# Kernel optimization log

Measured on AMD Instinct MI355X. Metric: run time of the kernel, lower is better.

The kernel has to match this reference:

```python
import jax, jax.numpy as jnp
import numpy as np

NEIGH = (3, 3, 3)  # attn_neighbourhood_size -> 27 one-hot impulse filters


def setup_inputs() -> dict:
    key = jax.random.key(0)
    b, h, d = 2, 8, 32
    H = W = D = 24
    x = jax.random.normal(key, (b, h, H * W * D, d), dtype=jnp.float32)
    return {"x": x, "height": H, "width": W, "depth": D}


def _localize(x, height, width, depth):
    # x: [b, h, N, d] with N = height*width*depth
    b, h, N, d = x.shape
    nh, nw, nd = NEIGH
    ph, pw, pd = (nh - 1) // 2, (nw - 1) // 2, (nd - 1) // 2
    # 'b h (i j k) d -> b h d i j k'
    y = x.reshape(b, h, height, width, depth, d).transpose(0, 1, 5, 2, 3, 4)
    yp = jnp.pad(y, ((0, 0), (0, 0), (0, 0), (ph, ph), (pw, pw), (pd, pd)))
    # conv3d with a unit impulse at (i,j,k) and 'same' padding is exactly the
    # shifted gather out[p] = x_padded[p + (i,j,k)]; emit the 27 shifts directly.
    slices = []
    for i in range(nh):
        for j in range(nw):
            for k in range(nd):
                slices.append(yp[..., i:i + height, j:j + width, k:k + depth])
    # [b, h, d, H, W, D, filter_n]
    out = jnp.stack(slices, axis=-1)
    fn = nh * nw * nd
    # '(b h d) filter_n i j k -> b h (i j k) filter_n d'
    out = out.reshape(b, h, d, N, fn).transpose(0, 1, 3, 4, 2)
    return out


def reference(x, height, width, depth):
    return _localize(x, height, width, depth)
```

## Files before the change

### kernel.cpp

```cpp
#include <hip/hip_runtime.h>


typedef float v4f __attribute__((ext_vector_type(4)));

constexpr int H = 24, W = 24, D = 24;
constexpr int N = H * W * D;
constexpr int FN = 27;
constexpr int BH = 16;
constexpr int N4_REAL = BH * N * FN * 8;

__global__ __launch_bounds__(256) void localize_kernel(
    const v4f* __restrict__ x4, v4f* __restrict__ out4) {
  int idx = blockIdx.x * 256 + threadIdx.x;

  int c4 = idx & 7;
  int t  = idx >> 3;
  int f  = t % FN;
  int t2 = t / FN;
  int n  = t2 % N;

  int ii  = n / (W * D);
  int rem = n % (W * D);
  int jj  = rem / D;
  int kk  = rem % D;

  int di = f / 9 - 1;
  int dj = (f / 3) % 3 - 1;
  int dk = f % 3 - 1;

  int si = ii + di, sj = jj + dj, sk = kk + dk;

  v4f v = (v4f)(0.0f);
  if ((unsigned)si < (unsigned)H && (unsigned)sj < (unsigned)W &&
      (unsigned)sk < (unsigned)D) {
    int delta = di * (W * D) + dj * D + dk;
    v = x4[(t2 + delta) * 8 + c4];
  }
  __builtin_nontemporal_store(v, &out4[idx]);
}

extern "C" void kernel_launch(void* const* d_in, const int* in_sizes, int n_in,
                              void* d_out, int out_size, void* d_ws, size_t ws_size,
                              hipStream_t stream) {
  (void)in_sizes; (void)n_in; (void)out_size; (void)d_ws; (void)ws_size;
  const v4f* x4 = (const v4f*)d_in[0];
  v4f* out4 = (v4f*)d_out;
  int blocks = N4_REAL / 256;
  localize_kernel<<<blocks, 256, 0, stream>>>(x4, out4);
}
```

Before: 802.7 us.

## Stage 3x3 neighbourhood rows in LDS per (bh,i,j) workgroup before scatter

Each workgroup now handles one (bh, i, j) row of depth D. It loads the nine padded source rows (with zero halos) into shared memory, then writes all 27 shifted copies for that row from LDS. The aim is to remove redundant, partly uncoalesced global reads, since each input element was previously read up to 27 times. The cost is an extra barrier and LDS traffic, and a workgroup count that drops to 9216 with a strided loop of about 21 iterations per thread.

```diff
diff --git a/kernel.cpp b/kernel.cpp
--- a/kernel.cpp
+++ b/kernel.cpp
@@ -7,36 +7,48 @@
 constexpr int N = H * W * D;
 constexpr int FN = 27;
 constexpr int BH = 16;
-constexpr int N4_REAL = BH * N * FN * 8;
+constexpr int PLEN = D + 2;
+constexpr int LDS_N4 = 9 * PLEN * 8;
+constexpr int OUT_N4 = D * FN * 8;
 
 __global__ __launch_bounds__(256) void localize_kernel(
     const v4f* __restrict__ x4, v4f* __restrict__ out4) {
-  int idx = blockIdx.x * 256 + threadIdx.x;
+  __shared__ v4f lds[LDS_N4];
+  const int tid = threadIdx.x;
+  const int wg  = blockIdx.x;
+  const int bh  = wg / (H * W);
+  const int rem = wg - bh * (H * W);
+  const int ii  = rem / W;
+  const int jj  = rem - ii * W;
 
-  int c4 = idx & 7;
-  int t  = idx >> 3;
-  int f  = t % FN;
-  int t2 = t / FN;
-  int n  = t2 % N;
+  for (int o = tid; o < LDS_N4; o += 256) {
+    int c4   = o & 7;
+    int r    = o >> 3;
+    int p    = r / PLEN;
+    int srck = r - p * PLEN;
+    int si   = ii + p / 3 - 1;
+    int sj   = jj + p % 3 - 1;
+    int sk   = srck - 1;
+    v4f v = (v4f)(0.0f);
+    if ((unsigned)si < (unsigned)H && (unsigned)sj < (unsigned)W &&
+        (unsigned)sk < (unsigned)D) {
+      v = x4[(((bh * H + si) * W + sj) * D + sk) * 8 + c4];
+    }
+    lds[o] = v;
+  }
+  __syncthreads();
 
-  int ii  = n / (W * D);
-  int rem = n % (W * D);
-  int jj  = rem / D;
-  int kk  = rem % D;
-
-  int di = f / 9 - 1;
-  int dj = (f / 3) % 3 - 1;
-  int dk = f % 3 - 1;
-
-  int si = ii + di, sj = jj + dj, sk = kk + dk;
-
-  v4f v = (v4f)(0.0f);
-  if ((unsigned)si < (unsigned)H && (unsigned)sj < (unsigned)W &&
-      (unsigned)sk < (unsigned)D) {
-    int delta = di * (W * D) + dj * D + dk;
-    v = x4[(t2 + delta) * 8 + c4];
+  const int base = (bh * N + ii * (W * D) + jj * D) * (FN * 8);
+  for (int o = tid; o < OUT_N4; o += 256) {
+    int c4   = o & 7;
+    int t    = o >> 3;
+    int f    = t % FN;
+    int kk   = t / FN;
+    int p    = f / 3;
+    int srck = kk + f % 3;
+    v4f v = lds[(p * PLEN + srck) * 8 + c4];
+    __builtin_nontemporal_store(v, &out4[base + o]);
   }
-  __builtin_nontemporal_store(v, &out4[idx]);
 }
 
 extern "C" void kernel_launch(void* const* d_in, const int* in_sizes, int n_in,
@@ -45,6 +57,6 @@
   (void)in_sizes; (void)n_in; (void)out_size; (void)d_ws; (void)ws_size;
   const v4f* x4 = (const v4f*)d_in[0];
   v4f* out4 = (v4f*)d_out;
-  int blocks = N4_REAL / 256;
+  int blocks = BH * H * W;
   localize_kernel<<<blocks, 256, 0, stream>>>(x4, out4);
 }
```

New measurement: 758.6 us. 5.5% less time.
